# Kernel optimization log

Hardware: AMD Instinct MI355X
Metric: run time of the kernel (lower is better)

Reference implementation:

```python
import jax, jax.numpy as jnp
import numpy as np

IN_FEATURE = 256
OUT_FEATURE = 128
ALPHA = 0.5  # LeakyReLU negative slope
NEG_BIG = -9e15


def setup_inputs() -> dict:
    key = jax.random.key(0)
    k1, k2, k3, k4 = jax.random.split(key, 4)
    N = 8192
    x = jax.random.normal(k1, (N, IN_FEATURE), dtype=jnp.float32)
    adj = jax.random.randint(k2, (N, N), 0, 2, dtype=jnp.int32)
    stdv = 1.0 / np.sqrt(OUT_FEATURE)
    W = jax.random.uniform(k3, (IN_FEATURE, OUT_FEATURE), dtype=jnp.float32,
                           minval=-stdv, maxval=stdv)
    a = jax.random.uniform(k4, (2 * OUT_FEATURE, 1), dtype=jnp.float32,
                           minval=-stdv, maxval=stdv)
    return {"input": x, "adj": adj, "W": W, "a": a}


def reference(input, adj, W, a):
    # h: [N, F_out]
    h = input @ W
    # Additive attention: cat([h_i, h_j]) @ a == h_i @ a1 + h_j @ a2
    a1 = a[:OUT_FEATURE, 0]   # [F_out]
    a2 = a[OUT_FEATURE:, 0]   # [F_out]
    f1 = h @ a1               # [N]  (row / source contribution)
    f2 = h @ a2               # [N]  (col / target contribution)
    e = jax.nn.leaky_relu(f1[:, None] + f2[None, :], negative_slope=ALPHA)  # [N, N]
    scores = jnp.where(adj > 0, e, NEG_BIG)
    attention = jax.nn.softmax(scores, axis=1)  # [N, N]
    h_prime = attention @ h                     # [N, F_out]
    return jax.nn.elu(h_prime)
```

## Files before the change

### kernel.cpp

```cpp
#include <hip/hip_runtime.h>

#define N_NODES 8192
#define IN_F 256
#define OUT_F 128
#define ALPHA 0.5f
#define JC 8
#define KCHUNK 1024
#define RK 128
#define ROUNDS 8
#define RSTEPS 4

using short8 = __attribute__((ext_vector_type(8))) short;
using f32x4  = __attribute__((ext_vector_type(4))) float;

__device__ __forceinline__ unsigned int f2bf(float f){
  unsigned int u = __float_as_uint(f);
  u += 0x7fffu + ((u >> 16) & 1u);
  return u >> 16;
}
__device__ __forceinline__ float bf2f(short s){
  return __uint_as_float(((unsigned int)(unsigned short)s) << 16);
}

__global__ __launch_bounds__(256) void k_hfp(const float* __restrict__ x,
                                             const float* __restrict__ W,
                                             const float* __restrict__ a,
                                             unsigned short* __restrict__ P,
                                             float* __restrict__ f1,
                                             float* __restrict__ f2){
  __shared__ float xs[16*IN_F];
  const int tid = threadIdx.x;
  const int bx = blockIdx.x;
  const int r0 = bx * 16;
  const float4* xg = (const float4*)(x + (size_t)r0*IN_F);
  float4* xl = (float4*)xs;
  #pragma unroll
  for(int i=0;i<4;i++) xl[tid + i*256] = xg[tid + i*256];
  __syncthreads();
  const int wave = tid >> 6, lane = tid & 63;
  float2 acc[4];
  #pragma unroll
  for(int j=0;j<4;j++){ acc[j].x = 0.f; acc[j].y = 0.f; }
  const float2* Wp = (const float2*)W;
  for(int k4=0;k4<IN_F;k4+=4){
    float4 xq[4];
    #pragma unroll
    for(int j=0;j<4;j++) xq[j] = *(const float4*)&xs[(wave*4+j)*IN_F + k4];
    #pragma unroll
    for(int kk=0;kk<4;kk++){
      float2 wv = Wp[(size_t)(k4+kk)*64 + lane];
      #pragma unroll
      for(int j=0;j<4;j++){
        float xv = kk==0?xq[j].x : kk==1?xq[j].y : kk==2?xq[j].z : xq[j].w;
        acc[j].x += xv*wv.x; acc[j].y += xv*wv.y;
      }
    }
  }
  float2 av1 = ((const float2*)a)[lane];
  float2 av2 = ((const float2*)(a + OUT_F))[lane];
  #pragma unroll
  for(int j=0;j<4;j++){
    float s1 = acc[j].x*av1.x + acc[j].y*av1.y;
    float s2 = acc[j].x*av2.x + acc[j].y*av2.y;
    #pragma unroll
    for(int off=32; off; off>>=1){
      s1 += __shfl_down(s1, off);
      s2 += __shfl_down(s2, off);
    }
    if(lane == 0){ f1[r0 + wave*4 + j] = s1; f2[r0 + wave*4 + j] = s2; }
  }
  __syncthreads();
  #pragma unroll
  for(int j=0;j<4;j++) *(float2*)&xs[(wave*4+j)*132 + lane*2] = acc[j];
  __syncthreads();
  const int kb = bx >> 1, half = bx & 1;
  const int c = tid >> 5, ql = (tid >> 4) & 1, n = tid & 15;
  short8 v;
  #pragma unroll
  for(int t=0;t<8;t++) v[t] = (short)f2bf(xs[(ql*8+t)*132 + c*16 + n]);
  *(short8*)(P + ((size_t)((kb*8 + c)*64 + half*32 + ql*16 + n))*8) = v;
}

__global__ __launch_bounds__(256, 3) void k_attn(const int* __restrict__ adj,
    const unsigned short* __restrict__ P,
    const float* __restrict__ f1, const float* __restrict__ f2,
    float* __restrict__ part, float* __restrict__ denp){
  __shared__ __align__(16) unsigned short Alds[64*RK];
  __shared__ __align__(16) short Blds[RK*OUT_F];
  __shared__ float f1s[64];
  const int tid = threadIdx.x;
  const int wave = tid >> 6, lane = tid & 63;
  const int m = lane & 15, q = lane >> 4;
  const int jc = blockIdx.x;
  const int r0b = blockIdx.y * 64;
  const int jb = jc * KCHUNK;
  const int kb0 = jc * (KCHUNK/32);
  const int srow = tid >> 5;
  const int sc0  = (tid & 31) * 4;
  const int swz  = ((((sc0 >> 3) ^ srow) << 4) | ((sc0 & 4) << 1));

  if(tid < 64) f1s[tid] = f1[r0b + tid];

  f32x4 acc0[8];
  #pragma unroll
  for(int c=0;c<8;c++) acc0[c] = (f32x4){0,0,0,0};
  float den0 = 0.f;

  const char* Ab = (const char*)Alds;
  char* Aw = (char*)Alds + swz;
  const int mw = m & 7;
  const int rg0 = wave*16 + m;

  __syncthreads();

  for(int rd=0; rd<ROUNDS; rd++){
    const int kbase = jb + rd*RK;
    const int4* Pb = (const int4*)(P + ((size_t)(kb0 + rd*4) << 12));
    int4* Bl4 = (int4*)Blds;
    #pragma unroll
    for(int i=0;i<8;i++) Bl4[i*256 + tid] = Pb[i*256 + tid];
    float4 fv = *(const float4*)(f2 + kbase + sc0);
    const char* ap = (const char*)adj + (((size_t)(r0b + srow)*N_NODES + kbase + sc0) << 2);
    #pragma unroll
    for(int i=0;i<8;i++){
      int4 av = *(const int4*)(ap + ((size_t)i*8*N_NODES << 2));
      float f1v = f1s[i*8 + srow];
      float t0 = f1v + fv.x, t1 = f1v + fv.y, t2 = f1v + fv.z, t3 = f1v + fv.w;
      t0 = t0 > 0.f ? t0 : ALPHA*t0;  t1 = t1 > 0.f ? t1 : ALPHA*t1;
      t2 = t2 > 0.f ? t2 : ALPHA*t2;  t3 = t3 > 0.f ? t3 : ALPHA*t3;
      float w0 = av.x > 0 ? __expf(t0) : 0.f;
      float w1 = av.y > 0 ? __expf(t1) : 0.f;
      float w2 = av.z > 0 ? __expf(t2) : 0.f;
      float w3 = av.w > 0 ? __expf(t3) : 0.f;
      uint2 pk;
      pk.x = f2bf(w0) | (f2bf(w1) << 16);
      pk.y = f2bf(w2) | (f2bf(w3) << 16);
      *(uint2*)(Aw + (i*8 + srow)*(RK*2)) = pk;
    }
    __syncthreads();
    #pragma unroll
    for(int s=0;s<RSTEPS;s++){
      const int gq = ((s*4 + q) ^ mw) << 4;
      short8 A0 = *(const short8*)(Ab + rg0*(RK*2) + gq);
      #pragma unroll
      for(int t=0;t<8;t++) den0 += bf2f(A0[t]);
      const short8* Bl = (const short8*)Blds + s*512 + lane;
      #pragma unroll
      for(int c=0;c<8;c++){
        short8 Bf = Bl[c*64];
        acc0[c] = __builtin_amdgcn_mfma_f32_16x16x32_bf16(A0, Bf, acc0[c], 0,0,0);
      }
    }
    __syncthreads();
  }

  den0 += __shfl_down(den0, 32); den0 += __shfl_down(den0, 16);
  const int r0w = r0b + wave*16;
  if(lane < 16) denp[(size_t)jc*N_NODES + r0w + lane] = den0;
  float* pp = part + (size_t)jc*N_NODES*OUT_F;
  #pragma unroll
  for(int c=0;c<8;c++){
    #pragma unroll
    for(int reg=0;reg<4;reg++)
      pp[(size_t)(r0w + q*4 + reg)*OUT_F + c*16 + m] = acc0[c][reg];
  }
}

__global__ __launch_bounds__(256) void k_out(const float* __restrict__ part,
    const float* __restrict__ denp, float* __restrict__ out){
  const int idx = blockIdx.x*256 + threadIdx.x;
  const int r = idx >> 5;
  float4 v = {0.f,0.f,0.f,0.f};
  float d = 0.f;
  #pragma unroll
  for(int p=0;p<JC;p++){
    float4 pv = *((const float4*)part + (size_t)p*(N_NODES*OUT_F/4) + idx);
    v.x += pv.x; v.y += pv.y; v.z += pv.z; v.w += pv.w;
    d += denp[(size_t)p*N_NODES + r];
  }
  float4 o;
  o.x = v.x/d; o.y = v.y/d; o.z = v.z/d; o.w = v.w/d;
  o.x = o.x>0.f ? o.x : (__expf(o.x)-1.f);
  o.y = o.y>0.f ? o.y : (__expf(o.y)-1.f);
  o.z = o.z>0.f ? o.z : (__expf(o.z)-1.f);
  o.w = o.w>0.f ? o.w : (__expf(o.w)-1.f);
  *((float4*)out + idx) = o;
}

extern "C" void kernel_launch(void* const* d_in, const int* in_sizes, int n_in,
                              void* d_out, int out_size, void* d_ws, size_t ws_size,
                              hipStream_t stream){
  const float* x   = (const float*)d_in[0];
  const int*   adj = (const int*)d_in[1];
  const float* W   = (const float*)d_in[2];
  const float* a   = (const float*)d_in[3];
  char* ws = (char*)d_ws;
  unsigned short* P = (unsigned short*)ws;
  float* f1         = (float*)(ws + (2u<<20));
  float* f2         = (float*)(ws + (2u<<20) + (32u<<10));
  float* part       = (float*)(ws + (4u<<20));
  float* denp       = (float*)(ws + (36u<<20));
  float* out        = (float*)d_out;

  k_hfp<<<512, 256, 0, stream>>>(x, W, a, P, f1, f2);
  k_attn<<<dim3(JC,128), 256, 0, stream>>>(adj, P, f1, f2, part, denp);
  k_out<<<(N_NODES*OUT_F)/4/256, 256, 0, stream>>>(part, denp, out);
}
```

Before: 400.2 us.

## Register-prefetch next round of adj and P tiles; halve column splits

The attention kernel's main loop now double-buffers in registers. While the current round's bf16 weights and MFMAs run, it loads the next round's P tile, adjacency ints and f2 values, which hides global memory latency. The column split drops from 8 to 4 chunks of 2048 with 16 rounds each, which halves the partial-sum traffic and the reduction work in k_out. In exchange it uses many more registers, so occupancy falls from 3 to 2 blocks per SIMD, and the grid has fewer blocks.

Measured after the change: 473.1 us. 1.18x slower.

```diff
diff --git a/kernel.cpp b/kernel.cpp
--- a/kernel.cpp
+++ b/kernel.cpp
@@ -4,10 +4,10 @@
 #define IN_F 256
 #define OUT_F 128
 #define ALPHA 0.5f
-#define JC 8
-#define KCHUNK 1024
+#define JC 4
+#define KCHUNK 2048
 #define RK 128
-#define ROUNDS 8
+#define ROUNDS 16
 #define RSTEPS 4
 
 using short8 = __attribute__((ext_vector_type(8))) short;
@@ -81,7 +81,7 @@
   *(short8*)(P + ((size_t)((kb*8 + c)*64 + half*32 + ql*16 + n))*8) = v;
 }
 
-__global__ __launch_bounds__(256, 3) void k_attn(const int* __restrict__ adj,
+__global__ __launch_bounds__(256, 2) void k_attn(const int* __restrict__ adj,
     const unsigned short* __restrict__ P,
     const float* __restrict__ f1, const float* __restrict__ f2,
     float* __restrict__ part, float* __restrict__ denp){
@@ -110,49 +110,73 @@
   char* Aw = (char*)Alds + swz;
   const int mw = m & 7;
   const int rg0 = wave*16 + m;
-
-  __syncthreads();
-
-  for(int rd=0; rd<ROUNDS; rd++){
-    const int kbase = jb + rd*RK;
-    const int4* Pb = (const int4*)(P + ((size_t)(kb0 + rd*4) << 12));
-    int4* Bl4 = (int4*)Blds;
-    #pragma unroll
-    for(int i=0;i<8;i++) Bl4[i*256 + tid] = Pb[i*256 + tid];
-    float4 fv = *(const float4*)(f2 + kbase + sc0);
-    const char* ap = (const char*)adj + (((size_t)(r0b + srow)*N_NODES + kbase + sc0) << 2);
-    #pragma unroll
-    for(int i=0;i<8;i++){
-      int4 av = *(const int4*)(ap + ((size_t)i*8*N_NODES << 2));
-      float f1v = f1s[i*8 + srow];
-      float t0 = f1v + fv.x, t1 = f1v + fv.y, t2 = f1v + fv.z, t3 = f1v + fv.w;
-      t0 = t0 > 0.f ? t0 : ALPHA*t0;  t1 = t1 > 0.f ? t1 : ALPHA*t1;
-      t2 = t2 > 0.f ? t2 : ALPHA*t2;  t3 = t3 > 0.f ? t3 : ALPHA*t3;
-      float w0 = av.x > 0 ? __expf(t0) : 0.f;
-      float w1 = av.y > 0 ? __expf(t1) : 0.f;
-      float w2 = av.z > 0 ? __expf(t2) : 0.f;
-      float w3 = av.w > 0 ? __expf(t3) : 0.f;
-      uint2 pk;
-      pk.x = f2bf(w0) | (f2bf(w1) << 16);
-      pk.y = f2bf(w2) | (f2bf(w3) << 16);
-      *(uint2*)(Aw + (i*8 + srow)*(RK*2)) = pk;
-    }
-    __syncthreads();
-    #pragma unroll
-    for(int s=0;s<RSTEPS;s++){
-      const int gq = ((s*4 + q) ^ mw) << 4;
-      short8 A0 = *(const short8*)(Ab + rg0*(RK*2) + gq);
-      #pragma unroll
-      for(int t=0;t<8;t++) den0 += bf2f(A0[t]);
-      const short8* Bl = (const short8*)Blds + s*512 + lane;
-      #pragma unroll
-      for(int c=0;c<8;c++){
-        short8 Bf = Bl[c*64];
-        acc0[c] = __builtin_amdgcn_mfma_f32_16x16x32_bf16(A0, Bf, acc0[c], 0,0,0);
-      }
-    }
-    __syncthreads();
-  }
+  int4* Bl4 = (int4*)Blds;
+  const char* apbase = (const char*)adj + (((size_t)(r0b + srow)*N_NODES + jb + sc0) << 2);
+
+  __syncthreads();
+
+  int4 bA[8], bB[8], aA[8], aB[8];
+  float4 fA, fB;
+  {
+    const int4* Pb = (const int4*)(P + ((size_t)kb0 << 12));
+    #pragma unroll
+    for(int i=0;i<8;i++) bA[i] = Pb[i*256 + tid];
+    #pragma unroll
+    for(int i=0;i<8;i++) aA[i] = *(const int4*)(apbase + ((size_t)i*8*N_NODES << 2));
+    fA = *(const float4*)(f2 + jb + sc0);
+  }
+
+#define RB(RD, AC, AN, BC, BN, FC, FN)                                          \
+  {                                                                             \
+    const int rdn = ((RD)+1 < ROUNDS) ? (RD)+1 : (RD);                          \
+    const int4* Pbn = (const int4*)(P + ((size_t)(kb0 + rdn*4) << 12));         \
+    _Pragma("unroll")                                                           \
+    for(int i=0;i<8;i++) BN[i] = Pbn[i*256 + tid];                              \
+    const char* apn = apbase + ((size_t)(rdn*RK) << 2);                         \
+    _Pragma("unroll")                                                           \
+    for(int i=0;i<8;i++) AN[i] = *(const int4*)(apn + ((size_t)i*8*N_NODES << 2)); \
+    FN = *(const float4*)(f2 + jb + rdn*RK + sc0);                              \
+    _Pragma("unroll")                                                           \
+    for(int i=0;i<8;i++) Bl4[i*256 + tid] = BC[i];                              \
+    _Pragma("unroll")                                                           \
+    for(int i=0;i<8;i++){                                                       \
+      int4 av = AC[i];                                                          \
+      float f1v = f1s[i*8 + srow];                                              \
+      float t0 = f1v + FC.x, t1 = f1v + FC.y, t2 = f1v + FC.z, t3 = f1v + FC.w; \
+      t0 = t0 > 0.f ? t0 : ALPHA*t0;  t1 = t1 > 0.f ? t1 : ALPHA*t1;            \
+      t2 = t2 > 0.f ? t2 : ALPHA*t2;  t3 = t3 > 0.f ? t3 : ALPHA*t3;            \
+      float w0 = av.x > 0 ? __expf(t0) : 0.f;                                   \
+      float w1 = av.y > 0 ? __expf(t1) : 0.f;                                   \
+      float w2 = av.z > 0 ? __expf(t2) : 0.f;                                   \
+      float w3 = av.w > 0 ? __expf(t3) : 0.f;                                   \
+      uint2 pk;                                                                 \
+      pk.x = f2bf(w0) | (f2bf(w1) << 16);                                       \
+      pk.y = f2bf(w2) | (f2bf(w3) << 16);                                       \
+      *(uint2*)(Aw + (i*8 + srow)*(RK*2)) = pk;                                 \
+    }                                                                           \
+    asm volatile("s_waitcnt lgkmcnt(0)" ::: "memory");                          \
+    __builtin_amdgcn_s_barrier();                                               \
+    _Pragma("unroll")                                                           \
+    for(int s=0;s<RSTEPS;s++){                                                  \
+      const int gq = ((s*4 + q) ^ mw) << 4;                                     \
+      short8 A0 = *(const short8*)(Ab + rg0*(RK*2) + gq);                       \
+      _Pragma("unroll")                                                         \
+      for(int t=0;t<8;t++) den0 += bf2f(A0[t]);                                 \
+      const short8* Bl = (const short8*)Blds + s*512 + lane;                    \
+      _Pragma("unroll")                                                         \
+      for(int c=0;c<8;c++){                                                     \
+        short8 Bf = Bl[c*64];                                                   \
+        acc0[c] = __builtin_amdgcn_mfma_f32_16x16x32_bf16(A0, Bf, acc0[c], 0,0,0); \
+      }                                                                         \
+    }                                                                           \
+    __builtin_amdgcn_s_barrier();                                               \
+  }
+
+  for(int rd2=0; rd2<ROUNDS; rd2+=2){
+    RB(rd2,   aA, aB, bA, bB, fA, fB)
+    RB(rd2+1, aB, aA, bB, bA, fB, fA)
+  }
+#undef RB
 
   den0 += __shfl_down(den0, 32); den0 += __shfl_down(den0, 16);
   const int r0w = r0b + wave*16;
@@ -199,7 +223,7 @@
   float* f1         = (float*)(ws + (2u<<20));
   float* f2         = (float*)(ws + (2u<<20) + (32u<<10));
   float* part       = (float*)(ws + (4u<<20));
-  float* denp       = (float*)(ws + (36u<<20));
+  float* denp       = (float*)(ws + (20u<<20));
   float* out        = (float*)d_out;
 
   k_hfp<<<512, 256, 0, stream>>>(x, W, a, P, f1, f2);
```
